# Kernel tuning notes

Measured on AMD Instinct MI355X. Metric: run time of the kernel, lower is better.

The kernel has to match this reference:

```python
import jax, jax.numpy as jnp
import numpy as np

B, N, D = 256, 50, 128
NEG = -9e15  # torch uses -9000000000000000.0
LEAKY_SLOPE = 0.2


def setup_inputs() -> dict:
    key = jax.random.key(0)
    ks = jax.random.split(key, 6)
    hidden = jax.random.normal(ks[0], (B, N, D), dtype=jnp.float32)
    adj = jax.random.randint(ks[1], (B, N, N), 0, 5)  # edge types 0..4
    a_0 = jax.random.normal(ks[2], (D, 1), dtype=jnp.float32) * 0.05
    a_1 = jax.random.normal(ks[3], (D, 1), dtype=jnp.float32) * 0.05
    a_2 = jax.random.normal(ks[4], (D, 1), dtype=jnp.float32) * 0.05
    a_3 = jax.random.normal(ks[5], (D, 1), dtype=jnp.float32) * 0.05
    return {"hidden": hidden, "adj": adj, "a_0": a_0, "a_1": a_1, "a_2": a_2, "a_3": a_3}


def reference(hidden, adj, a_0, a_1, a_2, a_3):
    # LocalAggregator.forward (typed-edge GAT over session graph).
    # Original builds a_input[b,i,j,:] = h[b,i,:]*h[b,j,:] (B,N,N,D) then
    # projects with 4 relation vectors a_k (D,1). We fuse: stack the 4
    # vectors and contract D in one einsum -> e[b,k,i,j].
    A = jnp.concatenate([a_0, a_1, a_2, a_3], axis=1)          # (D, 4)
    e = jnp.einsum('bid,bjd,dk->bkij', hidden, hidden, A)      # (B, 4, N, N)
    e = jax.nn.leaky_relu(e, negative_slope=LEAKY_SLOPE)
    # Per-edge-type masking: adj value v in {1..4} selects branch v-1,
    # anything else gets -9e15 (same chained torch.where semantics/order).
    scores = jnp.full_like(e[:, 0], NEG)                        # (B, N, N)
    scores = jnp.where(adj == 1, e[:, 0], scores)
    scores = jnp.where(adj == 2, e[:, 1], scores)
    scores = jnp.where(adj == 3, e[:, 2], scores)
    scores = jnp.where(adj == 4, e[:, 3], scores)
    attn = jax.nn.softmax(scores, axis=-1)                      # (B, N, N)
    return jnp.einsum('bij,bjd->bid', attn, hidden)             # (B, N, D)
```

## Files before the change

kernel.cpp:

```cpp
#include <hip/hip_runtime.h>
#include <stdint.h>

typedef __attribute__((ext_vector_type(8))) short short8;
typedef __attribute__((ext_vector_type(4))) float f32x4;

namespace {
constexpr int   kN     = 50;
constexpr int   kD     = 128;
constexpr float kNeg   = -9.0e15f;
constexpr float kSlope = 0.2f;
constexpr int   HS32   = 132;
constexpr int   HS16   = 136;
constexpr int   SS     = 68;
constexpr int   AS     = 36;
constexpr int   ADS    = 52;
}

union Pack8 { uint32_t u[4]; short8 s; };

__global__ __launch_bounds__(512)
void gat_v7_kernel(const float* __restrict__ hidden,
                   const int*   __restrict__ adj,
                   const float* __restrict__ a0,
                   const float* __restrict__ a1,
                   const float* __restrict__ a2,
                   const float* __restrict__ a3,
                   float* __restrict__ out)
{
    __shared__ float          Hf [kN * HS32];
    __shared__ unsigned short Hhi[64 * HS16];
    __shared__ unsigned short Hlo[64 * HS16];
    __shared__ float          Sa [32 * SS];
    __shared__ unsigned short At [64 * AS];
    __shared__ unsigned char  Ad [kN * ADS];

    const int b    = blockIdx.x >> 1;
    const int ih   = blockIdx.x & 1;
    const int tid  = threadIdx.x;
    const int lane = tid & 63;
    const int wid  = __builtin_amdgcn_readfirstlane(tid >> 6);
    const int g    = lane >> 4;
    const int f    = lane & 15;

    const float* __restrict__ hb   = hidden + (size_t)b * (kN * kD);
    const int*   __restrict__ adjb = adj    + (size_t)b * (kN * kN);
    float*       __restrict__ outb = out    + (size_t)b * (kN * kD);

    const float4* hg = reinterpret_cast<const float4*>(hb);
    #pragma unroll
    for (int it4 = 0; it4 < 4; ++it4) {
        const int idx = tid + it4 * 512;
        const int j   = idx >> 5;
        const int d4  = idx & 31;
        float4 v = make_float4(0.f, 0.f, 0.f, 0.f);
        if (j < kN) v = hg[j * 32 + d4];

        const uint32_t h0 = __float_as_uint(v.x) & 0xffff0000u;
        const uint32_t h1 = __float_as_uint(v.y) & 0xffff0000u;
        const uint32_t h2 = __float_as_uint(v.z) & 0xffff0000u;
        const uint32_t h3 = __float_as_uint(v.w) & 0xffff0000u;
        uint2 hiw;
        hiw.x = h1 | (h0 >> 16);
        hiw.y = h3 | (h2 >> 16);
        const float r0 = v.x - __uint_as_float(h0);
        const float r1 = v.y - __uint_as_float(h1);
        const float r2 = v.z - __uint_as_float(h2);
        const float r3 = v.w - __uint_as_float(h3);
        uint2 low;
        low.x = (__float_as_uint(r1) & 0xffff0000u) | (__float_as_uint(r0) >> 16);
        low.y = (__float_as_uint(r3) & 0xffff0000u) | (__float_as_uint(r2) >> 16);
        *reinterpret_cast<uint2*>(&Hhi[j * HS16 + 4 * d4]) = hiw;
        *reinterpret_cast<uint2*>(&Hlo[j * HS16 + 4 * d4]) = low;
        if (j < kN) *reinterpret_cast<float4*>(&Hf[j * HS32 + 4 * d4]) = v;
    }
    for (int idx = tid; idx < 625; idx += 512) {
        const int4 v = reinterpret_cast<const int4*>(adjb)[idx];
        const int e = 4 * idx;
        const int vv[4] = {v.x, v.y, v.z, v.w};
        #pragma unroll
        for (int p = 0; p < 4; ++p) {
            const int ee  = e + p;
            const int row = ee / kN;
            const int col = ee - kN * row;
            Ad[row * ADS + col] = (unsigned char)vv[p];
        }
    }
    __syncthreads();

    {
        const int jt   = wid & 3;
        const int itL  = wid >> 2;
        const int itG  = 2 * ih + itL;
        const int i0   = 16 * itG;
        const int irow = (i0 + f < kN) ? (i0 + f) : (kN - 1);
        const int jrow = 16 * jt + f;

        f32x4 acc[4];
        #pragma unroll
        for (int k = 0; k < 4; ++k) acc[k] = (f32x4){0.f, 0.f, 0.f, 0.f};

        const float* __restrict__ aks[4] = {a0, a1, a2, a3};

        #pragma unroll
        for (int ksl = 0; ksl < 4; ++ksl) {
            const int dofs = 32 * ksl + 8 * g;

            const float4 hA0 = *reinterpret_cast<const float4*>(&Hf[irow * HS32 + dofs]);
            const float4 hA1 = *reinterpret_cast<const float4*>(&Hf[irow * HS32 + dofs + 4]);
            const float ha[8] = {hA0.x, hA0.y, hA0.z, hA0.w, hA1.x, hA1.y, hA1.z, hA1.w};

            const short8 bh = *reinterpret_cast<const short8*>(&Hhi[jrow * HS16 + dofs]);
            const short8 bl = *reinterpret_cast<const short8*>(&Hlo[jrow * HS16 + dofs]);

            #pragma unroll
            for (int k = 0; k < 4; ++k) {
                const float4 av0 = *reinterpret_cast<const float4*>(aks[k] + dofs);
                const float4 av1 = *reinterpret_cast<const float4*>(aks[k] + dofs + 4);
                const float aa[8] = {av0.x, av0.y, av0.z, av0.w, av1.x, av1.y, av1.z, av1.w};
                Pack8 ph, pl;
                #pragma unroll
                for (int p = 0; p < 4; ++p) {
                    const float q0 = ha[2 * p]     * aa[2 * p];
                    const float q1 = ha[2 * p + 1] * aa[2 * p + 1];
                    const uint32_t b0 = __float_as_uint(q0) & 0xffff0000u;
                    const uint32_t b1 = __float_as_uint(q1) & 0xffff0000u;
                    ph.u[p] = b1 | (b0 >> 16);
                    const float s0 = q0 - __uint_as_float(b0);
                    const float s1 = q1 - __uint_as_float(b1);
                    pl.u[p] = (__float_as_uint(s1) & 0xffff0000u) | (__float_as_uint(s0) >> 16);
                }
                acc[k] = __builtin_amdgcn_mfma_f32_16x16x32_bf16(ph.s, bh, acc[k], 0, 0, 0);
                acc[k] = __builtin_amdgcn_mfma_f32_16x16x32_bf16(ph.s, bl, acc[k], 0, 0, 0);
                acc[k] = __builtin_amdgcn_mfma_f32_16x16x32_bf16(pl.s, bh, acc[k], 0, 0, 0);
            }
        }

        const int j = 16 * jt + f;
        #pragma unroll
        for (int reg = 0; reg < 4; ++reg) {
            const int iL = 16 * itL + 4 * g + reg;
            const int ii = 32 * ih + iL;
            if (ii < kN && j < kN) {
                const int kv = Ad[ii * ADS + j];
                const float val = (kv == 1) ? acc[0][reg]
                                : (kv == 2) ? acc[1][reg]
                                : (kv == 3) ? acc[2][reg]
                                : (kv == 4) ? acc[3][reg] : 0.f;
                const float lx = (val > 0.f) ? val : kSlope * val;
                Sa[iL * SS + j] = (kv >= 1 && kv <= 4) ? lx : kNeg;
            }
        }
    }
    __syncthreads();

    {
        const int icount = ih ? (kN - 32) : 32;
        #pragma unroll
        for (int t = 0; t < 4; ++t) {
            const int rL = wid + 8 * t;
            if (rL < icount) {
                const float s = (lane < kN) ? Sa[rL * SS + lane] : kNeg;
                float m = s;
                #pragma unroll
                for (int o = 32; o; o >>= 1) m = fmaxf(m, __shfl_xor(m, o));
                const float e = (lane < kN) ? __expf(s - m) : 0.f;
                float ts = e;
                #pragma unroll
                for (int o = 32; o; o >>= 1) ts += __shfl_xor(ts, o);
                uint32_t u = __float_as_uint(e / ts);
                u += 0x7fffu + ((u >> 16) & 1u);
                At[lane * AS + rL] = (unsigned short)(u >> 16);
            }
        }
    }
    __syncthreads();

    if (wid < 4) {
        const int itL = wid & 1;
        const int dh  = wid >> 1;
        const int i0L = 16 * itL;
        const int db  = 64 * dh + 4 * f;

        f32x4 o0 = {0.f, 0.f, 0.f, 0.f}, o1 = o0, o2 = o0, o3 = o0;
        #pragma unroll 5
        for (int j = 0; j < kN; ++j) {
            const float4  hv = *reinterpret_cast<const float4*>(&Hf[j * HS32 + db]);
            const ushort4 a4 = *reinterpret_cast<const ushort4*>(&At[j * AS + i0L + 4 * g]);
            const float av0 = __uint_as_float(((uint32_t)a4.x) << 16);
            const float av1 = __uint_as_float(((uint32_t)a4.y) << 16);
            const float av2 = __uint_as_float(((uint32_t)a4.z) << 16);
            const float av3 = __uint_as_float(((uint32_t)a4.w) << 16);
            o0.x += av0 * hv.x; o0.y += av0 * hv.y; o0.z += av0 * hv.z; o0.w += av0 * hv.w;
            o1.x += av1 * hv.x; o1.y += av1 * hv.y; o1.z += av1 * hv.z; o1.w += av1 * hv.w;
            o2.x += av2 * hv.x; o2.y += av2 * hv.y; o2.z += av2 * hv.z; o2.w += av2 * hv.w;
            o3.x += av3 * hv.x; o3.y += av3 * hv.y; o3.z += av3 * hv.z; o3.w += av3 * hv.w;
        }
        const int iiB = 32 * ih + i0L + 4 * g;
        if (iiB + 0 < kN) *reinterpret_cast<f32x4*>(&outb[(iiB + 0) * kD + db]) = o0;
        if (iiB + 1 < kN) *reinterpret_cast<f32x4*>(&outb[(iiB + 1) * kD + db]) = o1;
        if (iiB + 2 < kN) *reinterpret_cast<f32x4*>(&outb[(iiB + 2) * kD + db]) = o2;
        if (iiB + 3 < kN) *reinterpret_cast<f32x4*>(&outb[(iiB + 3) * kD + db]) = o3;
    }
}

extern "C" void kernel_launch(void* const* d_in, const int* in_sizes, int n_in,
                              void* d_out, int out_size, void* d_ws, size_t ws_size,
                              hipStream_t stream) {
    const float* hidden = reinterpret_cast<const float*>(d_in[0]);
    const int*   adjp   = reinterpret_cast<const int*>(d_in[1]);
    const float* a0     = reinterpret_cast<const float*>(d_in[2]);
    const float* a1     = reinterpret_cast<const float*>(d_in[3]);
    const float* a2     = reinterpret_cast<const float*>(d_in[4]);
    const float* a3     = reinterpret_cast<const float*>(d_in[5]);
    float*       outp   = reinterpret_cast<float*>(d_out);

    gat_v7_kernel<<<dim3(512), dim3(512), 0, stream>>>(
        hidden, adjp, a0, a1, a2, a3, outp);
}
```

Measured before the change: 20.09 us.

## Split score contraction over D across waves with LDS atomics, drop fp32 LDS copy

The score GEMM is repartitioned so that each wave owns one 32-wide D slice and all four j-tiles. Per-wave partial scores are summed into zeroed LDS with atomicAdd, and the mask and leaky-relu move into the softmax stage. The fp32 copy of hidden in LDS is removed: the A operand and the final aggregation read hidden straight from global memory, and the aggregation now uses all 8 waves on float2 slices. This cuts LDS footprint and idle waves in the last phase, at the cost of LDS atomics and repeated global (L2) reads of hidden.

```diff
diff --git a/kernel.cpp b/kernel.cpp
--- a/kernel.cpp
+++ b/kernel.cpp
@@ -9,7 +9,6 @@
 constexpr int   kD     = 128;
 constexpr float kNeg   = -9.0e15f;
 constexpr float kSlope = 0.2f;
-constexpr int   HS32   = 132;
 constexpr int   HS16   = 136;
 constexpr int   SS     = 68;
 constexpr int   AS     = 36;
@@ -19,7 +18,7 @@
 union Pack8 { uint32_t u[4]; short8 s; };
 
 __global__ __launch_bounds__(512)
-void gat_v7_kernel(const float* __restrict__ hidden,
+void gat_v9_kernel(const float* __restrict__ hidden,
                    const int*   __restrict__ adj,
                    const float* __restrict__ a0,
                    const float* __restrict__ a1,
@@ -27,7 +26,6 @@
                    const float* __restrict__ a3,
                    float* __restrict__ out)
 {
-    __shared__ float          Hf [kN * HS32];
     __shared__ unsigned short Hhi[64 * HS16];
     __shared__ unsigned short Hlo[64 * HS16];
     __shared__ float          Sa [32 * SS];
@@ -45,6 +43,22 @@
     const float* __restrict__ hb   = hidden + (size_t)b * (kN * kD);
     const int*   __restrict__ adjb = adj    + (size_t)b * (kN * kN);
     float*       __restrict__ outb = out    + (size_t)b * (kN * kD);
+
+    for (int idx = tid; idx < 544; idx += 512)
+        reinterpret_cast<float4*>(Sa)[idx] = make_float4(0.f, 0.f, 0.f, 0.f);
+
+    for (int idx = tid; idx < 625; idx += 512) {
+        const int4 v = reinterpret_cast<const int4*>(adjb)[idx];
+        const int e = 4 * idx;
+        const int vv[4] = {v.x, v.y, v.z, v.w};
+        #pragma unroll
+        for (int p = 0; p < 4; ++p) {
+            const int ee  = e + p;
+            const int row = ee / kN;
+            const int col = ee - kN * row;
+            Ad[row * ADS + col] = (unsigned char)vv[p];
+        }
+    }
 
     const float4* hg = reinterpret_cast<const float4*>(hb);
     #pragma unroll
@@ -71,83 +85,81 @@
         low.y = (__float_as_uint(r3) & 0xffff0000u) | (__float_as_uint(r2) >> 16);
         *reinterpret_cast<uint2*>(&Hhi[j * HS16 + 4 * d4]) = hiw;
         *reinterpret_cast<uint2*>(&Hlo[j * HS16 + 4 * d4]) = low;
-        if (j < kN) *reinterpret_cast<float4*>(&Hf[j * HS32 + 4 * d4]) = v;
-    }
-    for (int idx = tid; idx < 625; idx += 512) {
-        const int4 v = reinterpret_cast<const int4*>(adjb)[idx];
-        const int e = 4 * idx;
-        const int vv[4] = {v.x, v.y, v.z, v.w};
-        #pragma unroll
-        for (int p = 0; p < 4; ++p) {
-            const int ee  = e + p;
-            const int row = ee / kN;
-            const int col = ee - kN * row;
-            Ad[row * ADS + col] = (unsigned char)vv[p];
-        }
     }
     __syncthreads();
 
     {
-        const int jt   = wid & 3;
-        const int itL  = wid >> 2;
-        const int itG  = 2 * ih + itL;
-        const int i0   = 16 * itG;
+        const int itL = wid & 1;
+        const int kq  = wid >> 1;
+        const int i0  = 32 * ih + 16 * itL;
         const int irow = (i0 + f < kN) ? (i0 + f) : (kN - 1);
-        const int jrow = 16 * jt + f;
-
-        f32x4 acc[4];
-        #pragma unroll
-        for (int k = 0; k < 4; ++k) acc[k] = (f32x4){0.f, 0.f, 0.f, 0.f};
+        const int dofs = 32 * kq + 8 * g;
+
+        const float4 hA0 = *reinterpret_cast<const float4*>(hb + irow * kD + dofs);
+        const float4 hA1 = *reinterpret_cast<const float4*>(hb + irow * kD + dofs + 4);
+        const float ha[8] = {hA0.x, hA0.y, hA0.z, hA0.w, hA1.x, hA1.y, hA1.z, hA1.w};
 
         const float* __restrict__ aks[4] = {a0, a1, a2, a3};
-
-        #pragma unroll
-        for (int ksl = 0; ksl < 4; ++ksl) {
-            const int dofs = 32 * ksl + 8 * g;
-
-            const float4 hA0 = *reinterpret_cast<const float4*>(&Hf[irow * HS32 + dofs]);
-            const float4 hA1 = *reinterpret_cast<const float4*>(&Hf[irow * HS32 + dofs + 4]);
-            const float ha[8] = {hA0.x, hA0.y, hA0.z, hA0.w, hA1.x, hA1.y, hA1.z, hA1.w};
-
+        short8 qh[4], ql[4];
+        #pragma unroll
+        for (int k = 0; k < 4; ++k) {
+            const float4 av0 = *reinterpret_cast<const float4*>(aks[k] + dofs);
+            const float4 av1 = *reinterpret_cast<const float4*>(aks[k] + dofs + 4);
+            const float aa[8] = {av0.x, av0.y, av0.z, av0.w, av1.x, av1.y, av1.z, av1.w};
+            Pack8 ph, pl;
+            #pragma unroll
+            for (int p = 0; p < 4; ++p) {
+                const float q0 = ha[2 * p]     * aa[2 * p];
+                const float q1 = ha[2 * p + 1] * aa[2 * p + 1];
+                const uint32_t b0 = __float_as_uint(q0) & 0xffff0000u;
+                const uint32_t b1 = __float_as_uint(q1) & 0xffff0000u;
+                ph.u[p] = b1 | (b0 >> 16);
+                const float s0 = q0 - __uint_as_float(b0);
+                const float s1 = q1 - __uint_as_float(b1);
+                pl.u[p] = (__float_as_uint(s1) & 0xffff0000u) | (__float_as_uint(s0) >> 16);
+            }
+            qh[k] = ph.s;
+            ql[k] = pl.s;
+        }
+
+        f32x4 acc[4][4];
+        #pragma unroll
+        for (int jt = 0; jt < 4; ++jt)
+            #pragma unroll
+            for (int k = 0; k < 4; ++k) acc[jt][k] = (f32x4){0.f, 0.f, 0.f, 0.f};
+
+        #pragma unroll
+        for (int jt = 0; jt < 4; ++jt) {
+            const int jrow = 16 * jt + f;
             const short8 bh = *reinterpret_cast<const short8*>(&Hhi[jrow * HS16 + dofs]);
             const short8 bl = *reinterpret_cast<const short8*>(&Hlo[jrow * HS16 + dofs]);
-
             #pragma unroll
             for (int k = 0; k < 4; ++k) {
-                const float4 av0 = *reinterpret_cast<const float4*>(aks[k] + dofs);
-                const float4 av1 = *reinterpret_cast<const float4*>(aks[k] + dofs + 4);
-                const float aa[8] = {av0.x, av0.y, av0.z, av0.w, av1.x, av1.y, av1.z, av1.w};
-                Pack8 ph, pl;
+                acc[jt][k] = __builtin_amdgcn_mfma_f32_16x16x32_bf16(qh[k], bh, acc[jt][k], 0, 0, 0);
+                acc[jt][k] = __builtin_amdgcn_mfma_f32_16x16x32_bf16(qh[k], bl, acc[jt][k], 0, 0, 0);
+                acc[jt][k] = __builtin_amdgcn_mfma_f32_16x16x32_bf16(ql[k], bh, acc[jt][k], 0, 0, 0);
+            }
+        }
+
+        #pragma unroll
+        for (int jt = 0; jt < 4; ++jt) {
+            const int j = 16 * jt + f;
+            if (j < kN) {
                 #pragma unroll
-                for (int p = 0; p < 4; ++p) {
-                    const float q0 = ha[2 * p]     * aa[2 * p];
-                    const float q1 = ha[2 * p + 1] * aa[2 * p + 1];
-                    const uint32_t b0 = __float_as_uint(q0) & 0xffff0000u;
-                    const uint32_t b1 = __float_as_uint(q1) & 0xffff0000u;
-                    ph.u[p] = b1 | (b0 >> 16);
-                    const float s0 = q0 - __uint_as_float(b0);
-                    const float s1 = q1 - __uint_as_float(b1);
-                    pl.u[p] = (__float_as_uint(s1) & 0xffff0000u) | (__float_as_uint(s0) >> 16);
+                for (int reg = 0; reg < 4; ++reg) {
+                    const int iL = 16 * itL + 4 * g + reg;
+                    const int ii = 32 * ih + iL;
+                    if (ii < kN) {
+                        const int kv = Ad[ii * ADS + j];
+                        if (kv >= 1 && kv <= 4) {
+                            const float val = (kv == 1) ? acc[jt][0][reg]
+                                            : (kv == 2) ? acc[jt][1][reg]
+                                            : (kv == 3) ? acc[jt][2][reg]
+                                            :             acc[jt][3][reg];
+                            atomicAdd(&Sa[iL * SS + j], val);
+                        }
+                    }
                 }
-                acc[k] = __builtin_amdgcn_mfma_f32_16x16x32_bf16(ph.s, bh, acc[k], 0, 0, 0);
-                acc[k] = __builtin_amdgcn_mfma_f32_16x16x32_bf16(ph.s, bl, acc[k], 0, 0, 0);
-                acc[k] = __builtin_amdgcn_mfma_f32_16x16x32_bf16(pl.s, bh, acc[k], 0, 0, 0);
-            }
-        }
-
-        const int j = 16 * jt + f;
-        #pragma unroll
-        for (int reg = 0; reg < 4; ++reg) {
-            const int iL = 16 * itL + 4 * g + reg;
-            const int ii = 32 * ih + iL;
-            if (ii < kN && j < kN) {
-                const int kv = Ad[ii * ADS + j];
-                const float val = (kv == 1) ? acc[0][reg]
-                                : (kv == 2) ? acc[1][reg]
-                                : (kv == 3) ? acc[2][reg]
-                                : (kv == 4) ? acc[3][reg] : 0.f;
-                const float lx = (val > 0.f) ? val : kSlope * val;
-                Sa[iL * SS + j] = (kv >= 1 && kv <= 4) ? lx : kNeg;
             }
         }
     }
@@ -157,9 +169,16 @@
         const int icount = ih ? (kN - 32) : 32;
         #pragma unroll
         for (int t = 0; t < 4; ++t) {
-            const int rL = wid + 8 * t;
+            const int rL = 4 * wid + t;
             if (rL < icount) {
-                const float s = (lane < kN) ? Sa[rL * SS + lane] : kNeg;
+                const int ii = 32 * ih + rL;
+                int kv = 0;
+                if (lane < kN) kv = Ad[ii * ADS + lane];
+                float s = kNeg;
+                if (kv >= 1 && kv <= 4) {
+                    const float x = Sa[rL * SS + lane];
+                    s = (x > 0.f) ? x : kSlope * x;
+                }
                 float m = s;
                 #pragma unroll
                 for (int o = 32; o; o >>= 1) m = fmaxf(m, __shfl_xor(m, o));
@@ -169,37 +188,37 @@
                 for (int o = 32; o; o >>= 1) ts += __shfl_xor(ts, o);
                 uint32_t u = __float_as_uint(e / ts);
                 u += 0x7fffu + ((u >> 16) & 1u);
-                At[lane * AS + rL] = (unsigned short)(u >> 16);
+                if (lane < kN) At[lane * AS + rL] = (unsigned short)(u >> 16);
             }
         }
     }
     __syncthreads();
 
-    if (wid < 4) {
+    {
         const int itL = wid & 1;
-        const int dh  = wid >> 1;
+        const int dq  = wid >> 1;
         const int i0L = 16 * itL;
-        const int db  = 64 * dh + 4 * f;
-
-        f32x4 o0 = {0.f, 0.f, 0.f, 0.f}, o1 = o0, o2 = o0, o3 = o0;
+        const int db  = 32 * dq + 2 * f;
+
+        float2 o0 = {0.f, 0.f}, o1 = o0, o2 = o0, o3 = o0;
         #pragma unroll 5
         for (int j = 0; j < kN; ++j) {
-            const float4  hv = *reinterpret_cast<const float4*>(&Hf[j * HS32 + db]);
+            const float2  hv = *reinterpret_cast<const float2*>(hb + j * kD + db);
             const ushort4 a4 = *reinterpret_cast<const ushort4*>(&At[j * AS + i0L + 4 * g]);
             const float av0 = __uint_as_float(((uint32_t)a4.x) << 16);
             const float av1 = __uint_as_float(((uint32_t)a4.y) << 16);
             const float av2 = __uint_as_float(((uint32_t)a4.z) << 16);
             const float av3 = __uint_as_float(((uint32_t)a4.w) << 16);
-            o0.x += av0 * hv.x; o0.y += av0 * hv.y; o0.z += av0 * hv.z; o0.w += av0 * hv.w;
-            o1.x += av1 * hv.x; o1.y += av1 * hv.y; o1.z += av1 * hv.z; o1.w += av1 * hv.w;
-            o2.x += av2 * hv.x; o2.y += av2 * hv.y; o2.z += av2 * hv.z; o2.w += av2 * hv.w;
-            o3.x += av3 * hv.x; o3.y += av3 * hv.y; o3.z += av3 * hv.z; o3.w += av3 * hv.w;
+            o0.x += av0 * hv.x; o0.y += av0 * hv.y;
+            o1.x += av1 * hv.x; o1.y += av1 * hv.y;
+            o2.x += av2 * hv.x; o2.y += av2 * hv.y;
+            o3.x += av3 * hv.x; o3.y += av3 * hv.y;
         }
         const int iiB = 32 * ih + i0L + 4 * g;
-        if (iiB + 0 < kN) *reinterpret_cast<f32x4*>(&outb[(iiB + 0) * kD + db]) = o0;
-        if (iiB + 1 < kN) *reinterpret_cast<f32x4*>(&outb[(iiB + 1) * kD + db]) = o1;
-        if (iiB + 2 < kN) *reinterpret_cast<f32x4*>(&outb[(iiB + 2) * kD + db]) = o2;
-        if (iiB + 3 < kN) *reinterpret_cast<f32x4*>(&outb[(iiB + 3) * kD + db]) = o3;
+        if (iiB + 0 < kN) *reinterpret_cast<float2*>(&outb[(iiB + 0) * kD + db]) = o0;
+        if (iiB + 1 < kN) *reinterpret_cast<float2*>(&outb[(iiB + 1) * kD + db]) = o1;
+        if (iiB + 2 < kN) *reinterpret_cast<float2*>(&outb[(iiB + 2) * kD + db]) = o2;
+        if (iiB + 3 < kN) *reinterpret_cast<float2*>(&outb[(iiB + 3) * kD + db]) = o3;
     }
 }
 
@@ -214,6 +233,6 @@
     const float* a3     = reinterpret_cast<const float*>(d_in[5]);
     float*       outp   = reinterpret_cast<float*>(d_out);
 
-    gat_v7_kernel<<<dim3(512), dim3(512), 0, stream>>>(
+    gat_v9_kernel<<<dim3(512), dim3(512), 0, stream>>>(
         hidden, adjp, a0, a1, a2, a3, outp);
 }
```

Result: slower. 30.80 us (+53.3%).

## Give each wave a full row tile with register softmax and wave-private weights

Applied to the files above, without the earlier changes.

The kernel now uses one 256-thread block per batch instead of two 512-thread blocks that split the rows. Each wave owns 16 rows across all 50 columns. Scores stay in registers, so the softmax reduces with 16-lane shuffles, and the attention weights go to a per-wave shared buffer. This removes the shared score round-trips and two block-wide barriers, and it stops loading H twice per batch. In exchange there are half as many blocks (256 for 256 CUs), a larger accumulator array per wave, and every wave now runs the output GEMV, so register pressure and occupancy may suffer.

```diff
diff --git a/kernel.cpp b/kernel.cpp
--- a/kernel.cpp
+++ b/kernel.cpp
@@ -11,31 +11,28 @@
 constexpr float kSlope = 0.2f;
 constexpr int   HS32   = 132;
 constexpr int   HS16   = 136;
-constexpr int   SS     = 68;
-constexpr int   AS     = 36;
 constexpr int   ADS    = 52;
+constexpr int   PS     = 20;
 }
 
 union Pack8 { uint32_t u[4]; short8 s; };
 
-__global__ __launch_bounds__(512)
-void gat_v7_kernel(const float* __restrict__ hidden,
-                   const int*   __restrict__ adj,
-                   const float* __restrict__ a0,
-                   const float* __restrict__ a1,
-                   const float* __restrict__ a2,
-                   const float* __restrict__ a3,
-                   float* __restrict__ out)
+__global__ __launch_bounds__(256)
+void gat_v10_kernel(const float* __restrict__ hidden,
+                    const int*   __restrict__ adj,
+                    const float* __restrict__ a0,
+                    const float* __restrict__ a1,
+                    const float* __restrict__ a2,
+                    const float* __restrict__ a3,
+                    float* __restrict__ out)
 {
     __shared__ float          Hf [kN * HS32];
     __shared__ unsigned short Hhi[64 * HS16];
     __shared__ unsigned short Hlo[64 * HS16];
-    __shared__ float          Sa [32 * SS];
-    __shared__ unsigned short At [64 * AS];
     __shared__ unsigned char  Ad [kN * ADS];
-
-    const int b    = blockIdx.x >> 1;
-    const int ih   = blockIdx.x & 1;
+    __shared__ unsigned short Pw [4][64 * PS];
+
+    const int b    = blockIdx.x;
     const int tid  = threadIdx.x;
     const int lane = tid & 63;
     const int wid  = __builtin_amdgcn_readfirstlane(tid >> 6);
@@ -48,8 +45,8 @@
 
     const float4* hg = reinterpret_cast<const float4*>(hb);
     #pragma unroll
-    for (int it4 = 0; it4 < 4; ++it4) {
-        const int idx = tid + it4 * 512;
+    for (int it8 = 0; it8 < 8; ++it8) {
+        const int idx = tid + it8 * 256;
         const int j   = idx >> 5;
         const int d4  = idx & 31;
         float4 v = make_float4(0.f, 0.f, 0.f, 0.f);
@@ -73,7 +70,7 @@
         *reinterpret_cast<uint2*>(&Hlo[j * HS16 + 4 * d4]) = low;
         if (j < kN) *reinterpret_cast<float4*>(&Hf[j * HS32 + 4 * d4]) = v;
     }
-    for (int idx = tid; idx < 625; idx += 512) {
+    for (int idx = tid; idx < 625; idx += 256) {
         const int4 v = reinterpret_cast<const int4*>(adjb)[idx];
         const int e = 4 * idx;
         const int vv[4] = {v.x, v.y, v.z, v.w};
@@ -87,119 +84,128 @@
     }
     __syncthreads();
 
-    {
-        const int jt   = wid & 3;
-        const int itL  = wid >> 2;
-        const int itG  = 2 * ih + itL;
-        const int i0   = 16 * itG;
-        const int irow = (i0 + f < kN) ? (i0 + f) : (kN - 1);
-        const int jrow = 16 * jt + f;
-
-        f32x4 acc[4];
-        #pragma unroll
-        for (int k = 0; k < 4; ++k) acc[k] = (f32x4){0.f, 0.f, 0.f, 0.f};
-
-        const float* __restrict__ aks[4] = {a0, a1, a2, a3};
-
-        #pragma unroll
-        for (int ksl = 0; ksl < 4; ++ksl) {
-            const int dofs = 32 * ksl + 8 * g;
-
-            const float4 hA0 = *reinterpret_cast<const float4*>(&Hf[irow * HS32 + dofs]);
-            const float4 hA1 = *reinterpret_cast<const float4*>(&Hf[irow * HS32 + dofs + 4]);
-            const float ha[8] = {hA0.x, hA0.y, hA0.z, hA0.w, hA1.x, hA1.y, hA1.z, hA1.w};
-
+    const int i0   = 16 * wid;
+    const int irow = (i0 + f < kN) ? (i0 + f) : (kN - 1);
+
+    f32x4 acc[4][4];
+    #pragma unroll
+    for (int jt = 0; jt < 4; ++jt)
+        #pragma unroll
+        for (int k = 0; k < 4; ++k) acc[jt][k] = (f32x4){0.f, 0.f, 0.f, 0.f};
+
+    const float* __restrict__ aks[4] = {a0, a1, a2, a3};
+
+    #pragma unroll
+    for (int ksl = 0; ksl < 4; ++ksl) {
+        const int dofs = 32 * ksl + 8 * g;
+
+        const float4 hA0 = *reinterpret_cast<const float4*>(&Hf[irow * HS32 + dofs]);
+        const float4 hA1 = *reinterpret_cast<const float4*>(&Hf[irow * HS32 + dofs + 4]);
+        const float ha[8] = {hA0.x, hA0.y, hA0.z, hA0.w, hA1.x, hA1.y, hA1.z, hA1.w};
+
+        short8 qh[4], ql[4];
+        #pragma unroll
+        for (int k = 0; k < 4; ++k) {
+            const float4 av0 = *reinterpret_cast<const float4*>(aks[k] + dofs);
+            const float4 av1 = *reinterpret_cast<const float4*>(aks[k] + dofs + 4);
+            const float aa[8] = {av0.x, av0.y, av0.z, av0.w, av1.x, av1.y, av1.z, av1.w};
+            Pack8 ph, pl;
+            #pragma unroll
+            for (int p = 0; p < 4; ++p) {
+                const float q0 = ha[2 * p]     * aa[2 * p];
+                const float q1 = ha[2 * p + 1] * aa[2 * p + 1];
+                const uint32_t b0 = __float_as_uint(q0) & 0xffff0000u;
+                const uint32_t b1 = __float_as_uint(q1) & 0xffff0000u;
+                ph.u[p] = b1 | (b0 >> 16);
+                const float s0 = q0 - __uint_as_float(b0);
+                const float s1 = q1 - __uint_as_float(b1);
+                pl.u[p] = (__float_as_uint(s1) & 0xffff0000u) | (__float_as_uint(s0) >> 16);
+            }
+            qh[k] = ph.s;
+            ql[k] = pl.s;
+        }
+
+        #pragma unroll
+        for (int jt = 0; jt < 4; ++jt) {
+            const int jrow = 16 * jt + f;
             const short8 bh = *reinterpret_cast<const short8*>(&Hhi[jrow * HS16 + dofs]);
             const short8 bl = *reinterpret_cast<const short8*>(&Hlo[jrow * HS16 + dofs]);
-
             #pragma unroll
             for (int k = 0; k < 4; ++k) {
-                const float4 av0 = *reinterpret_cast<const float4*>(aks[k] + dofs);
-                const float4 av1 = *reinterpret_cast<const float4*>(aks[k] + dofs + 4);
-                const float aa[8] = {av0.x, av0.y, av0.z, av0.w, av1.x, av1.y, av1.z, av1.w};
-                Pack8 ph, pl;
-                #pragma unroll
-                for (int p = 0; p < 4; ++p) {
-                    const float q0 = ha[2 * p]     * aa[2 * p];
-                    const float q1 = ha[2 * p + 1] * aa[2 * p + 1];
-                    const uint32_t b0 = __float_as_uint(q0) & 0xffff0000u;
-                    const uint32_t b1 = __float_as_uint(q1) & 0xffff0000u;
-                    ph.u[p] = b1 | (b0 >> 16);
-                    const float s0 = q0 - __uint_as_float(b0);
-                    const float s1 = q1 - __uint_as_float(b1);
-                    pl.u[p] = (__float_as_uint(s1) & 0xffff0000u) | (__float_as_uint(s0) >> 16);
-                }
-                acc[k] = __builtin_amdgcn_mfma_f32_16x16x32_bf16(ph.s, bh, acc[k], 0, 0, 0);
-                acc[k] = __builtin_amdgcn_mfma_f32_16x16x32_bf16(ph.s, bl, acc[k], 0, 0, 0);
-                acc[k] = __builtin_amdgcn_mfma_f32_16x16x32_bf16(pl.s, bh, acc[k], 0, 0, 0);
+                acc[jt][k] = __builtin_amdgcn_mfma_f32_16x16x32_bf16(qh[k], bh, acc[jt][k], 0, 0, 0);
+                acc[jt][k] = __builtin_amdgcn_mfma_f32_16x16x32_bf16(qh[k], bl, acc[jt][k], 0, 0, 0);
+                acc[jt][k] = __builtin_amdgcn_mfma_f32_16x16x32_bf16(ql[k], bh, acc[jt][k], 0, 0, 0);
             }
         }
-
+    }
+
+    float s[4][4];
+    #pragma unroll
+    for (int jt = 0; jt < 4; ++jt) {
         const int j = 16 * jt + f;
         #pragma unroll
         for (int reg = 0; reg < 4; ++reg) {
-            const int iL = 16 * itL + 4 * g + reg;
-            const int ii = 32 * ih + iL;
-            if (ii < kN && j < kN) {
-                const int kv = Ad[ii * ADS + j];
-                const float val = (kv == 1) ? acc[0][reg]
-                                : (kv == 2) ? acc[1][reg]
-                                : (kv == 3) ? acc[2][reg]
-                                : (kv == 4) ? acc[3][reg] : 0.f;
-                const float lx = (val > 0.f) ? val : kSlope * val;
-                Sa[iL * SS + j] = (kv >= 1 && kv <= 4) ? lx : kNeg;
-            }
-        }
-    }
-    __syncthreads();
-
-    {
-        const int icount = ih ? (kN - 32) : 32;
-        #pragma unroll
-        for (int t = 0; t < 4; ++t) {
-            const int rL = wid + 8 * t;
-            if (rL < icount) {
-                const float s = (lane < kN) ? Sa[rL * SS + lane] : kNeg;
-                float m = s;
-                #pragma unroll
-                for (int o = 32; o; o >>= 1) m = fmaxf(m, __shfl_xor(m, o));
-                const float e = (lane < kN) ? __expf(s - m) : 0.f;
-                float ts = e;
-                #pragma unroll
-                for (int o = 32; o; o >>= 1) ts += __shfl_xor(ts, o);
-                uint32_t u = __float_as_uint(e / ts);
-                u += 0x7fffu + ((u >> 16) & 1u);
-                At[lane * AS + rL] = (unsigned short)(u >> 16);
-            }
-        }
-    }
-    __syncthreads();
-
-    if (wid < 4) {
-        const int itL = wid & 1;
-        const int dh  = wid >> 1;
-        const int i0L = 16 * itL;
-        const int db  = 64 * dh + 4 * f;
-
+            const int ii  = i0 + 4 * g + reg;
+            const int iic = (ii < kN) ? ii : (kN - 1);
+            int kv = 0;
+            if (j < kN) kv = Ad[iic * ADS + j];
+            const float x = (kv == 1) ? acc[jt][0][reg]
+                          : (kv == 2) ? acc[jt][1][reg]
+                          : (kv == 3) ? acc[jt][2][reg]
+                          : (kv == 4) ? acc[jt][3][reg] : 0.f;
+            const float lx = (x > 0.f) ? x : kSlope * x;
+            s[jt][reg] = (kv >= 1 && kv <= 4) ? lx : kNeg;
+        }
+    }
+
+    #pragma unroll
+    for (int reg = 0; reg < 4; ++reg) {
+        float m = fmaxf(fmaxf(s[0][reg], s[1][reg]), fmaxf(s[2][reg], s[3][reg]));
+        #pragma unroll
+        for (int o = 1; o < 16; o <<= 1) m = fmaxf(m, __shfl_xor(m, o));
+
+        float e[4];
+        float t = 0.f;
+        #pragma unroll
+        for (int jt = 0; jt < 4; ++jt) {
+            const int j = 16 * jt + f;
+            e[jt] = (j < kN) ? __expf(s[jt][reg] - m) : 0.f;
+            t += e[jt];
+        }
+        #pragma unroll
+        for (int o = 1; o < 16; o <<= 1) t += __shfl_xor(t, o);
+
+        const float inv = 1.0f / t;
+        #pragma unroll
+        for (int jt = 0; jt < 4; ++jt) {
+            uint32_t u = __float_as_uint(e[jt] * inv);
+            u += 0x7fffu + ((u >> 16) & 1u);
+            Pw[wid][(16 * jt + f) * PS + 4 * g + reg] = (unsigned short)(u >> 16);
+        }
+    }
+
+    #pragma unroll
+    for (int dh = 0; dh < 2; ++dh) {
+        const int db = 64 * dh + 4 * f;
         f32x4 o0 = {0.f, 0.f, 0.f, 0.f}, o1 = o0, o2 = o0, o3 = o0;
         #pragma unroll 5
         for (int j = 0; j < kN; ++j) {
             const float4  hv = *reinterpret_cast<const float4*>(&Hf[j * HS32 + db]);
-            const ushort4 a4 = *reinterpret_cast<const ushort4*>(&At[j * AS + i0L + 4 * g]);
-            const float av0 = __uint_as_float(((uint32_t)a4.x) << 16);
-            const float av1 = __uint_as_float(((uint32_t)a4.y) << 16);
-            const float av2 = __uint_as_float(((uint32_t)a4.z) << 16);
-            const float av3 = __uint_as_float(((uint32_t)a4.w) << 16);
+            const ushort4 p4 = *reinterpret_cast<const ushort4*>(&Pw[wid][j * PS + 4 * g]);
+            const float av0 = __uint_as_float(((uint32_t)p4.x) << 16);
+            const float av1 = __uint_as_float(((uint32_t)p4.y) << 16);
+            const float av2 = __uint_as_float(((uint32_t)p4.z) << 16);
+            const float av3 = __uint_as_float(((uint32_t)p4.w) << 16);
             o0.x += av0 * hv.x; o0.y += av0 * hv.y; o0.z += av0 * hv.z; o0.w += av0 * hv.w;
             o1.x += av1 * hv.x; o1.y += av1 * hv.y; o1.z += av1 * hv.z; o1.w += av1 * hv.w;
             o2.x += av2 * hv.x; o2.y += av2 * hv.y; o2.z += av2 * hv.z; o2.w += av2 * hv.w;
             o3.x += av3 * hv.x; o3.y += av3 * hv.y; o3.z += av3 * hv.z; o3.w += av3 * hv.w;
         }
-        const int iiB = 32 * ih + i0L + 4 * g;
-        if (iiB + 0 < kN) *reinterpret_cast<f32x4*>(&outb[(iiB + 0) * kD + db]) = o0;
-        if (iiB + 1 < kN) *reinterpret_cast<f32x4*>(&outb[(iiB + 1) * kD + db]) = o1;
-        if (iiB + 2 < kN) *reinterpret_cast<f32x4*>(&outb[(iiB + 2) * kD + db]) = o2;
-        if (iiB + 3 < kN) *reinterpret_cast<f32x4*>(&outb[(iiB + 3) * kD + db]) = o3;
+        const int rbase = i0 + 4 * g;
+        if (rbase + 0 < kN) *reinterpret_cast<f32x4*>(&outb[(rbase + 0) * kD + db]) = o0;
+        if (rbase + 1 < kN) *reinterpret_cast<f32x4*>(&outb[(rbase + 1) * kD + db]) = o1;
+        if (rbase + 2 < kN) *reinterpret_cast<f32x4*>(&outb[(rbase + 2) * kD + db]) = o2;
+        if (rbase + 3 < kN) *reinterpret_cast<f32x4*>(&outb[(rbase + 3) * kD + db]) = o3;
     }
 }
 
@@ -214,6 +220,6 @@
     const float* a3     = reinterpret_cast<const float*>(d_in[5]);
     float*       outp   = reinterpret_cast<float*>(d_out);
 
-    gat_v7_kernel<<<dim3(512), dim3(512), 0, stream>>>(
+    gat_v10_kernel<<<dim3(256), dim3(256), 0, stream>>>(
         hidden, adjp, a0, a1, a2, a3, outp);
 }
```

Measured after the change: 18.33 us. 1.1x faster.
